# Performance work log

Measured on AMD Instinct MI355X. Metric: run time of the kernel, lower is better.

The kernel has to match this reference:

```python
import jax, jax.numpy as jnp
import numpy as np

B, T, E, H, D = 2, 2048, 1024, 16, 64
ROPE_BASE = 10000.0


def project(x, k):
    # Lift to Lorentz hyperboloid with curvature magnitude K=exp(k): <lx,lx>_L = -K
    K = jnp.exp(k)
    x0 = jnp.sqrt(K + jnp.sum(x * x, axis=-1, keepdims=True))
    return jnp.concatenate([x0, x], axis=-1)


def layer_norm(x, w, b, eps=1e-5):
    m = jnp.mean(x, axis=-1, keepdims=True)
    v = jnp.mean((x - m) ** 2, axis=-1, keepdims=True)
    return (x - m) * jax.lax.rsqrt(v + eps) * w + b


def setup_inputs() -> dict:
    key = jax.random.key(0)
    ks = jax.random.split(key, 8)
    s = 0.02
    return dict(
        x=jax.random.normal(ks[0], (B, T, E), jnp.float32),
        block_curvature=jnp.asarray(1.0, jnp.float32),
        mlp_curvature=jnp.asarray(1.0, jnp.float32),
        attn_curvatures=jnp.ones((1, H, 1, 1), jnp.float32),
        w_qkv=jax.random.normal(ks[1], (E + 1, 3 * E), jnp.float32) * s,
        w_attn_proj=jax.random.normal(ks[2], ((D + 1) * H, E), jnp.float32) * s,
        b_attn_proj=jnp.zeros((E,), jnp.float32),
        w_mlp_expand=jax.random.normal(ks[3], (E + 1, 4 * E + 3), jnp.float32) * s,
        b_mlp_expand=jnp.zeros((4 * E + 3,), jnp.float32),
        w_mlp_shrink=jax.random.normal(ks[4], (4 * (E + 1), E), jnp.float32) * s,
        b_mlp_shrink=jnp.zeros((E,), jnp.float32),
        ln_w=jnp.ones((E,), jnp.float32),
        ln_b=jnp.zeros((E,), jnp.float32),
    )


def _block(x, block_curvature, mlp_curvature, attn_curvatures, w_qkv,
           w_attn_proj, b_attn_proj, w_mlp_expand, b_mlp_expand,
           w_mlp_shrink, b_mlp_shrink, ln_w, ln_b):
    Bq, Tq = x.shape[0], x.shape[1]
    lx = project(x, block_curvature)  # (B,T,E+1)

    def block_norm(l):
        return project(layer_norm(l[..., 1:], ln_w, ln_b), block_curvature)

    def skip(l, f):  # hyperbolic skip: add space parts, re-lift
        return project(l[..., 1:] + f[..., 1:], block_curvature)

    def attn(l):
        qkv = l @ w_qkv  # (B,T,3E)
        q, k, v = jnp.split(qkv, 3, axis=-1)
        q = q.reshape(Bq, Tq, H, D)
        k = k.reshape(Bq, Tq, H, D)
        v = v.reshape(Bq, Tq, H, D)
        half = D // 2
        inv_freq = 1.0 / (ROPE_BASE ** (jnp.arange(0, D, 2, dtype=jnp.float32) / D))
        freqs = jnp.arange(Tq, dtype=jnp.float32)[:, None] * inv_freq[None, :]
        cos = jnp.cos(freqs)[None, :, None, :]  # (1,T,1,D/2)
        sin = jnp.sin(freqs)[None, :, None, :]

        def rope(t):
            t1, t2 = t[..., :half], t[..., half:]
            return jnp.concatenate([t1 * cos + t2 * sin, -t1 * sin + t2 * cos], axis=-1)

        q = rope(q).transpose(0, 2, 1, 3)  # (B,H,T,D)
        k = rope(k).transpose(0, 2, 1, 3)
        v = v.transpose(0, 2, 1, 3)
        K = jnp.exp(attn_curvatures)  # (1,H,1,1) per-head curvature
        qt = jnp.sqrt(K + jnp.sum(q * q, axis=-1, keepdims=True))  # time coord (B,H,T,1)
        kt = jnp.sqrt(K + jnp.sum(k * k, axis=-1, keepdims=True))
        lv = project(v, attn_curvatures)  # (B,H,T,D+1)
        # Lorentz inner product without materializing (B,H,T,T,D+1)
        inner = jnp.einsum('bhtd,bhsd->bhts', q, k) - qt * jnp.swapaxes(kt, -1, -2)
        ratio = jnp.maximum(-inner / K, 1.0 + 1e-7)
        dis = jnp.sqrt(K) * jnp.arccosh(ratio)  # (B,H,T,T)
        causal = jnp.tril(jnp.ones((Tq, Tq), dtype=bool))
        w = jnp.where(causal, -dis, -jnp.inf)  # neg_dis attention weight + causal bias
        aw = jax.nn.softmax(w, axis=-1)
        o = jnp.einsum('bhts,bhse->bhte', aw, lv)  # (B,H,T,D+1)
        lnorm2 = o[..., :1] ** 2 - jnp.sum(o[..., 1:] ** 2, axis=-1, keepdims=True)
        hn = jnp.sqrt(jnp.maximum(lnorm2, 1e-12))  # Lorentz norm
        o = o * jnp.sqrt(K) / hn  # renormalize back onto hyperboloid
        o = o.transpose(0, 2, 1, 3).reshape(Bq, Tq, H * (D + 1))
        return project(o @ w_attn_proj + b_attn_proj, block_curvature)

    def mlp(l):
        h = project(l @ w_mlp_expand + b_mlp_expand, mlp_curvature)[..., 1:]  # (B,T,4E+3)
        h = jax.nn.gelu(h, approximate=False)
        h = project(h, mlp_curvature)  # (B,T,4(E+1))
        return project(h @ w_mlp_shrink + b_mlp_shrink, block_curvature)

    lx = skip(lx, attn(block_norm(lx)))
    lx = skip(lx, mlp(block_norm(lx)))
    return lx


def reference(x, block_curvature, mlp_curvature, attn_curvatures, w_qkv,
              w_attn_proj, b_attn_proj, w_mlp_expand, b_mlp_expand,
              w_mlp_shrink, b_mlp_shrink, ln_w, ln_b):
    return _block(x, block_curvature, mlp_curvature, attn_curvatures, w_qkv,
                  w_attn_proj, b_attn_proj, w_mlp_expand, b_mlp_expand,
                  w_mlp_shrink, b_mlp_shrink, ln_w, ln_b)
```

## Files before the change

### kernel.cpp

```cpp
#include <hip/hip_runtime.h>
#include <math.h>

#define MM   4096
#define TT   2048
#define HH   16

typedef __bf16 bf16x8 __attribute__((ext_vector_type(8)));
typedef float f32x4 __attribute__((ext_vector_type(4)));

__device__ __forceinline__ void g2l16(const void* g, void* l) {
    __builtin_amdgcn_global_load_lds(
        (__attribute__((address_space(1))) void*)g,
        (__attribute__((address_space(3))) void*)l, 16, 0, 0);
}

#if __has_builtin(__builtin_amdgcn_exp2f)
__device__ __forceinline__ float fexp2(float x) { return __builtin_amdgcn_exp2f(x); }
#else
__device__ __forceinline__ float fexp2(float x) { return exp2f(x); }
#endif
#if __has_builtin(__builtin_amdgcn_logf)
__device__ __forceinline__ float flog2(float x) { return __builtin_amdgcn_logf(x); }
#else
__device__ __forceinline__ float flog2(float x) { return log2f(x); }
#endif
#if __has_builtin(__builtin_amdgcn_sqrtf)
__device__ __forceinline__ float fsqrt_(float x) { return __builtin_amdgcn_sqrtf(x); }
#else
__device__ __forceinline__ float fsqrt_(float x) { return sqrtf(x); }
#endif
#if __has_builtin(__builtin_amdgcn_rcpf)
__device__ __forceinline__ float frcp_(float x) { return __builtin_amdgcn_rcpf(x); }
#else
__device__ __forceinline__ float frcp_(float x) { return 1.0f / x; }
#endif
#if __has_builtin(__builtin_amdgcn_rsqf)
__device__ __forceinline__ float frsq_(float x) { return __builtin_amdgcn_rsqf(x); }
#else
__device__ __forceinline__ float frsq_(float x) { return rsqrtf(x); }
#endif

__device__ __forceinline__ float blockSum256(float v, volatile float* sb) {
    int lane = threadIdx.x & 63, w = threadIdx.x >> 6;
#pragma unroll
    for (int o = 32; o; o >>= 1) v += __shfl_xor(v, o);
    if (lane == 0) sb[w] = v;
    __syncthreads();
    v = sb[0] + sb[1] + sb[2] + sb[3];
    __syncthreads();
    return v;
}

__global__ __launch_bounds__(256) void block_norm_bf_k(
    const float* __restrict__ in, int ld,
    __bf16* __restrict__ out,
    const float* __restrict__ lw, const float* __restrict__ lb,
    const float* __restrict__ curv)
{
    int row = blockIdx.x;
    const float* x = in + (size_t)row * ld;
    __bf16* o = out + (size_t)row * 1056;
    __shared__ float sb[4];
    int tid = threadIdx.x;
    float v[4]; float s1 = 0.f, s2 = 0.f;
#pragma unroll
    for (int r = 0; r < 4; r++) {
        float t = x[tid + 256 * r];
        v[r] = t; s1 += t; s2 += t * t;
    }
    s1 = blockSum256(s1, sb);
    s2 = blockSum256(s2, sb);
    float mean = s1 * (1.f / 1024.f);
    float var  = s2 * (1.f / 1024.f) - mean * mean;
    float rs = rsqrtf(var + 1e-5f);
    float y[4]; float ssq = 0.f;
#pragma unroll
    for (int r = 0; r < 4; r++) {
        int i = tid + 256 * r;
        float t = (v[r] - mean) * rs * lw[i] + lb[i];
        y[r] = t; ssq += t * t;
    }
    ssq = blockSum256(ssq, sb);
#pragma unroll
    for (int r = 0; r < 4; r++) o[1 + tid + 256 * r] = (__bf16)y[r];
    if (tid == 0) o[0] = (__bf16)sqrtf(expf(*curv) + ssq);
    if (tid < 31) o[1025 + tid] = (__bf16)0.f;
}

__global__ __launch_bounds__(256) void row_x0_k(
    float* __restrict__ buf, int stride, int n, const float* __restrict__ curv)
{
    int row = blockIdx.x;
    float* base = buf + (size_t)row * stride;
    __shared__ float sb[4];
    float s = 0.f;
    for (int i = threadIdx.x; i < n; i += 256) { float t = base[1 + i]; s += t * t; }
    s = blockSum256(s, sb);
    if (threadIdx.x == 0) base[0] = sqrtf(expf(*curv) + s);
}

__global__ __launch_bounds__(256) void row_x0_bf_k(
    __bf16* __restrict__ buf, const float* __restrict__ curv)
{
    int row = blockIdx.x;
    __bf16* base = buf + (size_t)row * 4128;
    __shared__ float sb[4];
    float s = 0.f;
    for (int i = threadIdx.x; i < 4099; i += 256) { float t = (float)base[1 + i]; s += t * t; }
    s = blockSum256(s, sb);
    if (threadIdx.x == 0) base[0] = (__bf16)sqrtf(expf(*curv) + s);
    if (threadIdx.x < 28) base[4100 + threadIdx.x] = (__bf16)0.f;
}

__global__ __launch_bounds__(256) void wt_k(
    const float* __restrict__ W, int K, int N,
    __bf16* __restrict__ Wt, int Kp)
{
    __shared__ float s[32][33];
    int tx = threadIdx.x & 31, ty = threadIdx.x >> 5;
    int k0 = blockIdx.x * 32, n0 = blockIdx.y * 32;
#pragma unroll
    for (int r = 0; r < 4; r++) {
        int k = k0 + ty + 8 * r, n = n0 + tx;
        s[ty + 8 * r][tx] = (k < K && n < N) ? W[(size_t)k * N + n] : 0.f;
    }
    __syncthreads();
#pragma unroll
    for (int r = 0; r < 4; r++) {
        int n = n0 + ty + 8 * r, k = k0 + tx;
        if (n < N) Wt[(size_t)n * Kp + k] = (__bf16)s[tx][ty + 8 * r];
    }
}

template<bool BIAS, bool GELU, bool SKIP, bool OUTBF>
__global__ __launch_bounds__(256) void mgemm_k(
    const __bf16* __restrict__ A, int lda,
    const __bf16* __restrict__ Bt, int ldb,
    const float* __restrict__ bias,
    const float* __restrict__ skip, int ldskip,
    void* __restrict__ Cout, int ldc,
    int N, int Kp)
{
    __shared__ __bf16 sA[128 * 32];
    __shared__ __bf16 sB[128 * 32];
    int tid = threadIdx.x;
    int w = tid >> 6, lane = tid & 63;
    int m0 = blockIdx.y * 128, n0 = blockIdx.x * 128;
    const __bf16* Ab = A + (size_t)m0 * lda;
    const __bf16* Bb = Bt + (size_t)n0 * ldb;

    f32x4 zero = {0.f, 0.f, 0.f, 0.f};
    f32x4 acc[4][4];
#pragma unroll
    for (int i = 0; i < 4; i++)
#pragma unroll
        for (int j = 0; j < 4; j++) acc[i][j] = zero;

    int mw = (w & 1) * 64, nw = (w >> 1) * 64;
    int lr = lane & 15, lq = lane >> 4;
    int fko = lq * 8;

    int r1 = tid >> 2, kk1 = (tid & 3) * 8;
    int r2 = (tid + 256) >> 2, kk2 = (tid & 3) * 8;
    __bf16* lA1 = &sA[(size_t)(w * 64) * 8];
    __bf16* lA2 = &sA[(size_t)(256 + w * 64) * 8];
    __bf16* lB1 = &sB[(size_t)(w * 64) * 8];
    __bf16* lB2 = &sB[(size_t)(256 + w * 64) * 8];

    for (int k0 = 0; k0 < Kp; k0 += 32) {
        g2l16(Ab + (size_t)r1 * lda + k0 + kk1, lA1);
        g2l16(Ab + (size_t)r2 * lda + k0 + kk2, lA2);
        g2l16(Bb + (size_t)r1 * ldb + k0 + kk1, lB1);
        g2l16(Bb + (size_t)r2 * ldb + k0 + kk2, lB2);
        __syncthreads();
        bf16x8 af[4], bf[4];
#pragma unroll
        for (int i = 0; i < 4; i++) af[i] = *(const bf16x8*)&sA[(mw + i * 16 + lr) * 32 + fko];
#pragma unroll
        for (int j = 0; j < 4; j++) bf[j] = *(const bf16x8*)&sB[(nw + j * 16 + lr) * 32 + fko];
#pragma unroll
        for (int i = 0; i < 4; i++)
#pragma unroll
            for (int j = 0; j < 4; j++)
                acc[i][j] = __builtin_amdgcn_mfma_f32_16x16x32_bf16(af[i], bf[j], acc[i][j], 0, 0, 0);
        __syncthreads();
    }

#pragma unroll
    for (int j = 0; j < 4; j++) {
        int n = n0 + nw + j * 16 + lr;
        if (n < N) {
            float bv = BIAS ? bias[n] : 0.f;
#pragma unroll
            for (int i = 0; i < 4; i++) {
#pragma unroll
                for (int r = 0; r < 4; r++) {
                    int m = m0 + mw + i * 16 + lq * 4 + r;
                    float v = acc[i][j][r] + bv;
                    if (GELU) v = 0.5f * v * (1.f + erff(v * 0.70710678118654752f));
                    if (SKIP) v += skip[(size_t)m * ldskip + n];
                    if (OUTBF) ((__bf16*)Cout)[(size_t)m * ldc + n] = (__bf16)v;
                    else       ((float*)Cout)[(size_t)m * ldc + n] = v;
                }
            }
        }
    }
}

template<bool BIAS, bool GELU, bool SKIP>
__global__ __launch_bounds__(256) void mgemm64_k(
    const __bf16* __restrict__ A, int lda,
    const __bf16* __restrict__ Bt, int ldb,
    const float* __restrict__ bias,
    const float* __restrict__ skip, int ldskip,
    float* __restrict__ Cout, int ldc,
    int N, int Kp)
{
    __shared__ __bf16 sA[128 * 32];
    __shared__ __bf16 sB[64 * 32];
    int tid = threadIdx.x;
    int w = tid >> 6, lane = tid & 63;
    int m0 = blockIdx.y * 128, n0 = blockIdx.x * 64;
    const __bf16* Ab = A + (size_t)m0 * lda;
    const __bf16* Bb = Bt + (size_t)n0 * ldb;

    f32x4 zero = {0.f, 0.f, 0.f, 0.f};
    f32x4 acc[4][2];
#pragma unroll
    for (int i = 0; i < 4; i++) { acc[i][0] = zero; acc[i][1] = zero; }

    int mw = (w & 1) * 64, nw = (w >> 1) * 32;
    int lr = lane & 15, lq = lane >> 4;
    int fko = lq * 8;

    int rA = tid >> 2, kkA = (tid & 3) * 8;
    __bf16* lA1 = &sA[(size_t)(w * 64) * 8];
    __bf16* lA2 = &sA[(size_t)(256 + w * 64) * 8];
    __bf16* lB  = &sB[(size_t)(w * 64) * 8];

    for (int k0 = 0; k0 < Kp; k0 += 32) {
        g2l16(Ab + (size_t)rA * lda + k0 + kkA, lA1);
        g2l16(Ab + (size_t)(rA + 64) * lda + k0 + kkA, lA2);
        g2l16(Bb + (size_t)rA * ldb + k0 + kkA, lB);
        __syncthreads();
        bf16x8 af[4], bf[2];
#pragma unroll
        for (int i = 0; i < 4; i++) af[i] = *(const bf16x8*)&sA[(mw + i * 16 + lr) * 32 + fko];
#pragma unroll
        for (int j = 0; j < 2; j++) bf[j] = *(const bf16x8*)&sB[(nw + j * 16 + lr) * 32 + fko];
#pragma unroll
        for (int i = 0; i < 4; i++)
#pragma unroll
            for (int j = 0; j < 2; j++)
                acc[i][j] = __builtin_amdgcn_mfma_f32_16x16x32_bf16(af[i], bf[j], acc[i][j], 0, 0, 0);
        __syncthreads();
    }

#pragma unroll
    for (int j = 0; j < 2; j++) {
        int n = n0 + nw + j * 16 + lr;
        if (n < N) {
            float bv = BIAS ? bias[n] : 0.f;
#pragma unroll
            for (int i = 0; i < 4; i++) {
#pragma unroll
                for (int r = 0; r < 4; r++) {
                    int m = m0 + mw + i * 16 + lq * 4 + r;
                    float v = acc[i][j][r] + bv;
                    if (GELU) v = 0.5f * v * (1.f + erff(v * 0.70710678118654752f));
                    if (SKIP) v += skip[(size_t)m * ldskip + n];
                    Cout[(size_t)m * ldc + n] = v;
                }
            }
        }
    }
}

__global__ __launch_bounds__(256) void rope_k(
    float* __restrict__ QKV, const float* __restrict__ curv,
    float* __restrict__ qt, float* __restrict__ kt,
    __bf16* __restrict__ Kb, __bf16* __restrict__ Obf)
{
    int row = blockIdx.x;
    int b = row >> 11, t = row & (TT - 1);
    int wv = threadIdx.x >> 6, d = threadIdx.x & 63;
    int j = d & 31;
    float fr = (float)t * powf(10000.0f, -(float)(2 * j) / 64.0f);
    float cv = cosf(fr), sv = sinf(fr);
    float sgn = (d < 32) ? sv : -sv;
    for (int h = wv; h < HH; h += 4) {
        float Kh = expf(curv[h]);
        float* base = QKV + (size_t)row * 3072 + h * 64;
        float q = base[d], k = base[1024 + d];
        float qp = __shfl_xor(q, 32);
        float kp = __shfl_xor(k, 32);
        float qr = q * cv + qp * sgn;
        float kr = k * cv + kp * sgn;
        base[d] = qr;
        size_t oidx = ((size_t)(b * HH + h) * TT + t);
        Kb[oidx * 64 + d] = (__bf16)kr;
        float sq = qr * qr, sk = kr * kr;
#pragma unroll
        for (int o = 32; o; o >>= 1) {
            sq += __shfl_xor(sq, o);
            sk += __shfl_xor(sk, o);
        }
        if (d == 0) {
            qt[oidx] = sqrtf(Kh + sq);
            kt[oidx] = sqrtf(Kh + sk);
        }
    }
    if (threadIdx.x < 16) Obf[(size_t)row * 1056 + 1040 + threadIdx.x] = (__bf16)0.f;
}

__global__ __launch_bounds__(256) void vtrans_k(
    const float* __restrict__ QKV, const float* __restrict__ curv,
    __bf16* __restrict__ Vtb, float* __restrict__ vt)
{
    __shared__ float sT[64 * 65];
    int bh = blockIdx.y; int h = bh & (HH - 1); int b = bh >> 4;
    int t0 = blockIdx.x * 64;
    int tid = threadIdx.x, w = tid >> 6, lane = tid & 63;
    float Kh = expf(curv[h]);
    const float* vbase = QKV + (size_t)(b * TT + t0) * 3072 + 2048 + h * 64;
#pragma unroll 4
    for (int i = 0; i < 16; i++) {
        int tr = w * 16 + i;
        float v = vbase[(size_t)tr * 3072 + lane];
        sT[lane * 65 + tr] = v;
        float s = v * v;
#pragma unroll
        for (int o = 32; o; o >>= 1) s += __shfl_xor(s, o);
        if (lane == 0) vt[(size_t)bh * TT + t0 + tr] = sqrtf(Kh + s);
    }
    __syncthreads();
    int d = tid >> 2, seg = tid & 3;
    const float* r = &sT[d * 65 + seg * 16];
    bf16x8 o0, o1;
#pragma unroll
    for (int i = 0; i < 8; i++) { o0[i] = (__bf16)r[i]; o1[i] = (__bf16)r[8 + i]; }
    __bf16* dst = Vtb + ((size_t)bh * 64 + d) * TT + t0 + seg * 16;
    *(bf16x8*)dst = o0;
    *(bf16x8*)(dst + 8) = o1;
}

__global__ __launch_bounds__(256, 4) void flash_k(
    const float* __restrict__ QKV,
    const __bf16* __restrict__ Kb, const __bf16* __restrict__ Vtb,
    const float* __restrict__ qt, const float* __restrict__ kt,
    const float* __restrict__ vt,
    const float* __restrict__ curv,
    __bf16* __restrict__ O)
{
    __shared__ __bf16 sK[4096];
    __shared__ __bf16 sVt[4096];
    __shared__ __bf16 sP[4 * 16 * 72];
    __shared__ float skt[64], svt[64];

    int bh = blockIdx.x; int h = bh & (HH - 1); int b = bh >> 4;
    int pi = blockIdx.y;
    float Kh = expf(curv[h]);
    float sqKh = sqrtf(Kh), msqK = -sqKh, invKh = 1.0f / Kh;
    const float* tok = QKV + (size_t)b * TT * 3072 + h * 64;
    const char* KbB = (const char*)Kb + (size_t)bh * TT * 128;
    const char* VtB = (const char*)Vtb + (size_t)bh * 64 * (TT * 2);
    const float* qtp = qt + (size_t)bh * TT;
    const float* ktp = kt + (size_t)bh * TT;
    const float* vtp = vt + (size_t)bh * TT;

    int tid = threadIdx.x;
    int w = tid >> 6, lane = tid & 63;
    int m = lane & 15, quad = lane >> 4;
    int qA = pi * 32, qB = (63 - pi) * 32;
    int myBase = (w < 2) ? (qA + 16 * w) : (qB + 16 * (w - 2));
    int myJmax = (myBase + 15) >> 6;
    int blockJmax = (qB + 31) >> 6;
    __bf16* sPw = &sP[w * 16 * 72];

    bf16x8 qhi[2], qlo[2];
    {
        const float* qrow = tok + (size_t)(myBase + m) * 3072;
#pragma unroll
        for (int ks = 0; ks < 2; ks++) {
            const float* s = qrow + quad * 8 + 32 * ks;
            float4 f0 = *(const float4*)s;
            float4 f1 = *(const float4*)(s + 4);
            float fa[8] = {f0.x, f0.y, f0.z, f0.w, f1.x, f1.y, f1.z, f1.w};
#pragma unroll
            for (int jj = 0; jj < 8; jj++) {
                __bf16 hv = (__bf16)fa[jj];
                qhi[ks][jj] = hv;
                qlo[ks][jj] = (__bf16)(fa[jj] - (float)hv);
            }
        }
    }
    float qtv[4]; int qg[4];
#pragma unroll
    for (int r = 0; r < 4; r++) { qg[r] = myBase + quad * 4 + r; qtv[r] = qtp[qg[r]]; }

    f32x4 zero = {0.f, 0.f, 0.f, 0.f};
    f32x4 accO[4];
#pragma unroll
    for (int nt = 0; nt < 4; nt++) accO[nt] = zero;
    float lsumr[4] = {}, o0r[4] = {};

    char* sKb  = (char*)sK  + w * 1024;
    char* sVb  = (char*)sVt + w * 1024;

    for (int j = 0; j <= blockJmax; ++j) {
        int sb = j << 6;
        __syncthreads();
        {
            const char* kg = KbB + (size_t)(sb + lane) * 128 + w * 16;
            g2l16(kg,      sKb);
            g2l16(kg + 64, sKb + 4096);
            const char* vg = VtB + (size_t)lane * (TT * 2) + sb * 2 + w * 16;
            g2l16(vg,      sVb);
            g2l16(vg + 64, sVb + 4096);
        }
        if (tid < 64) skt[tid] = ktp[sb + tid];
        else if (tid < 128) svt[tid - 64] = vtp[sb + tid - 64];
        __syncthreads();

        if (j > myJmax) continue;

        f32x4 accS[4];
#pragma unroll
        for (int nt = 0; nt < 4; nt++) accS[nt] = zero;
#pragma unroll
        for (int nt = 0; nt < 4; nt++) {
#pragma unroll
            for (int ksp = 0; ksp < 2; ksp++) {
                bf16x8 bk = *(const bf16x8*)&sK[((ksp * 4 + quad) * 64 + nt * 16 + m) * 8];
                accS[nt] = __builtin_amdgcn_mfma_f32_16x16x32_bf16(qhi[ksp], bk, accS[nt], 0, 0, 0);
                accS[nt] = __builtin_amdgcn_mfma_f32_16x16x32_bf16(qlo[ksp], bk, accS[nt], 0, 0, 0);
            }
        }
#pragma unroll
        for (int nt = 0; nt < 4; nt++) {
            int col = nt * 16 + m;
            int sglob = sb + col;
            float ktv = skt[col], vtv = svt[col];
#pragma unroll
            for (int r = 0; r < 4; r++) {
                float dot = accS[nt][r];
                float rdiff = fmaf(qtv[r], ktv, -dot);
                float ratio = fmaxf(rdiff * invKh, 1.0f + 1e-7f);
                float y = ratio + fsqrt_(fmaf(ratio, ratio, -1.0f));
                float pv = fexp2(msqK * flog2(y));
                float p = (sglob <= qg[r]) ? pv : 0.0f;
                lsumr[r] += p;
                o0r[r] = fmaf(p, vtv, o0r[r]);
                sPw[(quad * 4 + r) * 72 + col] = (__bf16)p;
            }
        }
        __asm__ volatile("s_waitcnt lgkmcnt(0)" ::: "memory");
#pragma unroll
        for (int ksp = 0; ksp < 2; ksp++) {
            bf16x8 aP = *(const bf16x8*)&sPw[m * 72 + ksp * 32 + quad * 8];
#pragma unroll
            for (int nt = 0; nt < 4; nt++) {
                bf16x8 bV = *(const bf16x8*)&sVt[((ksp * 4 + quad) * 64 + nt * 16 + m) * 8];
                accO[nt] = __builtin_amdgcn_mfma_f32_16x16x32_bf16(aP, bV, accO[nt], 0, 0, 0);
            }
        }
    }

#pragma unroll
    for (int r = 0; r < 4; r++) {
#pragma unroll
        for (int off = 1; off < 16; off <<= 1) {
            lsumr[r] += __shfl_xor(lsumr[r], off);
            o0r[r]   += __shfl_xor(o0r[r], off);
        }
    }
#pragma unroll
    for (int r = 0; r < 4; r++) {
        float inv = frcp_(lsumr[r]);
        float o0f = o0r[r] * inv;
        float ov[4]; float part = 0.f;
#pragma unroll
        for (int nt = 0; nt < 4; nt++) { float t = accO[nt][r] * inv; ov[nt] = t; part += t * t; }
        part += __shfl_xor(part, 1);
        part += __shfl_xor(part, 2);
        part += __shfl_xor(part, 4);
        part += __shfl_xor(part, 8);
        float scale = sqKh * frsq_(fmaxf(o0f * o0f - part, 1e-12f));
        size_t orow = (size_t)(b * TT + qg[r]) * 1056 + h * 65;
        if (m == 0) O[orow] = (__bf16)(o0f * scale);
#pragma unroll
        for (int nt = 0; nt < 4; nt++) O[orow + 1 + nt * 16 + m] = (__bf16)(ov[nt] * scale);
    }
}

extern "C" void kernel_launch(void* const* d_in, const int* in_sizes, int n_in,
                              void* d_out, int out_size, void* d_ws, size_t ws_size,
                              hipStream_t stream) {
    const float* x    = (const float*)d_in[0];
    const float* bc   = (const float*)d_in[1];
    const float* mc   = (const float*)d_in[2];
    const float* ac   = (const float*)d_in[3];
    const float* w_qkv = (const float*)d_in[4];
    const float* w_ap  = (const float*)d_in[5];
    const float* b_ap  = (const float*)d_in[6];
    const float* w_me  = (const float*)d_in[7];
    const float* b_me  = (const float*)d_in[8];
    const float* w_ms  = (const float*)d_in[9];
    const float* b_ms  = (const float*)d_in[10];
    const float* lnw  = (const float*)d_in[11];
    const float* lnb  = (const float*)d_in[12];
    float* out = (float*)d_out;
    float* ws  = (float*)d_ws;

    float* R      = ws;
    float* qkvbuf = R;
    float* X2     = R;
    __bf16* h_bf  = (__bf16*)(R + 4194304);
    float* p      = R + 12648448;
    __bf16* ln_bf = (__bf16*)p;  p += 2162688;
    __bf16* o_bf  = (__bf16*)p;  p += 2162688;
    __bf16* qkvT  = (__bf16*)p;  p += 1622016;
    __bf16* apT   = (__bf16*)p;  p += 540672;
    float*  meT_f = p;           p += 2164272;
    float*  msT_f = p;           p += 2113536;
    float* Qt = p;               p += 2 * HH * TT;
    float* Kt = p;               p += 2 * HH * TT;
    float* Vt = p;
    __bf16* meT = (__bf16*)meT_f;
    __bf16* msT = (__bf16*)msT_f;
    __bf16* Kb  = (__bf16*)meT_f;
    __bf16* Vtb = (__bf16*)msT_f;

    wt_k<<<dim3(33, 96),  256, 0, stream>>>(w_qkv, 1025, 3072, qkvT, 1056);
    wt_k<<<dim3(33, 32),  256, 0, stream>>>(w_ap,  1040, 1024, apT,  1056);

    block_norm_bf_k<<<MM, 256, 0, stream>>>(x, 1024, ln_bf, lnw, lnb, bc);
    mgemm_k<false, false, false, false><<<dim3(24, 32), 256, 0, stream>>>(
        ln_bf, 1056, qkvT, 1056, nullptr, nullptr, 0, qkvbuf, 3072, 3072, 1056);
    rope_k<<<MM, 256, 0, stream>>>(qkvbuf, ac, Qt, Kt, Kb, o_bf);
    vtrans_k<<<dim3(32, 32), 256, 0, stream>>>(qkvbuf, ac, Vtb, Vt);
    flash_k<<<dim3(2 * HH, 32), 256, 0, stream>>>(qkvbuf, Kb, Vtb, Qt, Kt, Vt, ac, o_bf);
    wt_k<<<dim3(33, 129), 256, 0, stream>>>(w_me,  1025, 4099, meT, 1056);
    wt_k<<<dim3(129, 32), 256, 0, stream>>>(w_ms,  4100, 1024, msT, 4128);
    mgemm64_k<true, false, true><<<dim3(16, 32), 256, 0, stream>>>(
        o_bf, 1056, apT, 1056, b_ap, x, 1024, X2, 1024, 1024, 1056);
    block_norm_bf_k<<<MM, 256, 0, stream>>>(X2, 1024, ln_bf, lnw, lnb, bc);
    mgemm_k<true, true, false, true><<<dim3(33, 32), 256, 0, stream>>>(
        ln_bf, 1056, meT, 1056, b_me, nullptr, 0, (void*)(h_bf + 1), 4128, 4099, 1056);
    row_x0_bf_k<<<MM, 256, 0, stream>>>(h_bf, mc);
    mgemm64_k<true, false, true><<<dim3(16, 32), 256, 0, stream>>>(
        h_bf, 4128, msT, 4128, b_ms, X2, 1024, out + 1, 1025, 1024, 4128);
    row_x0_k<<<MM, 256, 0, stream>>>(out, 1025, 1024, bc);
}
```

Measured before the change: 531.8 us.

## Replace 128x128 GEMM with double-buffered 256x256 swizzled MFMA kernel

Replaces the 128x128 single-buffered bf16 MFMA GEMM with a 512-thread 256x256-tile kernel. The new kernel uses a K-step of 64, double-buffered LDS prefetch via global_load_lds, an XOR-swizzled LDS layout, and setprio around the MFMA bursts. Leading dimensions are padded to multiples of 64 (1088, 4224) to fit the wider K-step, so the workspace offsets change. The 3 leftover MLP-expand columns (4096-4098) are computed by a small dot-product kernel fused into the x0 row reduction, so the big GEMM grid tiles N evenly. The aim is more data reuse and latency hiding in the QKV and MLP-expand GEMMs, at the cost of higher LDS and register use and extra padding traffic.

```diff
diff --git a/kernel.cpp b/kernel.cpp
--- a/kernel.cpp
+++ b/kernel.cpp
@@ -53,13 +53,13 @@
 
 __global__ __launch_bounds__(256) void block_norm_bf_k(
     const float* __restrict__ in, int ld,
-    __bf16* __restrict__ out,
+    __bf16* __restrict__ out, int ldo,
     const float* __restrict__ lw, const float* __restrict__ lb,
     const float* __restrict__ curv)
 {
     int row = blockIdx.x;
     const float* x = in + (size_t)row * ld;
-    __bf16* o = out + (size_t)row * 1056;
+    __bf16* o = out + (size_t)row * ldo;
     __shared__ float sb[4];
     int tid = threadIdx.x;
     float v[4]; float s1 = 0.f, s2 = 0.f;
@@ -84,7 +84,7 @@
 #pragma unroll
     for (int r = 0; r < 4; r++) o[1 + tid + 256 * r] = (__bf16)y[r];
     if (tid == 0) o[0] = (__bf16)sqrtf(expf(*curv) + ssq);
-    if (tid < 31) o[1025 + tid] = (__bf16)0.f;
+    if (tid < ldo - 1025) o[1025 + tid] = (__bf16)0.f;
 }
 
 __global__ __launch_bounds__(256) void row_x0_k(
@@ -99,17 +99,48 @@
     if (threadIdx.x == 0) base[0] = sqrtf(expf(*curv) + s);
 }
 
-__global__ __launch_bounds__(256) void row_x0_bf_k(
-    __bf16* __restrict__ buf, const float* __restrict__ curv)
+__global__ __launch_bounds__(256) void row_x0_tail_k(
+    __bf16* __restrict__ h,
+    const __bf16* __restrict__ ln,
+    const __bf16* __restrict__ Bt,
+    const float* __restrict__ bias,
+    const float* __restrict__ curv)
 {
     int row = blockIdx.x;
-    __bf16* base = buf + (size_t)row * 4128;
+    __bf16* base = h + (size_t)row * 4224;
+    const __bf16* lnr = ln + (size_t)row * 1088;
+    const __bf16* B0 = Bt + (size_t)4096 * 1088;
+    const __bf16* B1 = Bt + (size_t)4097 * 1088;
+    const __bf16* B2 = Bt + (size_t)4098 * 1088;
     __shared__ float sb[4];
+    float d0 = 0.f, d1 = 0.f, d2 = 0.f;
+    for (int i = threadIdx.x; i < 1088; i += 256) {
+        float a = (float)lnr[i];
+        d0 += a * (float)B0[i];
+        d1 += a * (float)B1[i];
+        d2 += a * (float)B2[i];
+    }
+    d0 = blockSum256(d0, sb);
+    d1 = blockSum256(d1, sb);
+    d2 = blockSum256(d2, sb);
+    float t3[3] = {d0 + bias[4096], d1 + bias[4097], d2 + bias[4098]};
+    float ssq_t = 0.f;
+#pragma unroll
+    for (int j = 0; j < 3; j++) {
+        float v = t3[j];
+        v = 0.5f * v * (1.f + erff(v * 0.70710678118654752f));
+        t3[j] = v; ssq_t += v * v;
+    }
+    if (threadIdx.x == 0) {
+        base[1 + 4096] = (__bf16)t3[0];
+        base[1 + 4097] = (__bf16)t3[1];
+        base[1 + 4098] = (__bf16)t3[2];
+    }
     float s = 0.f;
-    for (int i = threadIdx.x; i < 4099; i += 256) { float t = (float)base[1 + i]; s += t * t; }
-    s = blockSum256(s, sb);
+    for (int i = threadIdx.x; i < 4096; i += 256) { float t = (float)base[1 + i]; s += t * t; }
+    s = blockSum256(s, sb) + ssq_t;
     if (threadIdx.x == 0) base[0] = (__bf16)sqrtf(expf(*curv) + s);
-    if (threadIdx.x < 28) base[4100 + threadIdx.x] = (__bf16)0.f;
+    if (threadIdx.x < 124) base[4100 + threadIdx.x] = (__bf16)0.f;
 }
 
 __global__ __launch_bounds__(256) void wt_k(
@@ -132,73 +163,155 @@
     }
 }
 
-template<bool BIAS, bool GELU, bool SKIP, bool OUTBF>
-__global__ __launch_bounds__(256) void mgemm_k(
+template<bool BIAS, bool GELU, bool OUTBF>
+__global__ __launch_bounds__(512, 2) void mgemm256_k(
     const __bf16* __restrict__ A, int lda,
-    const __bf16* __restrict__ Bt, int ldb,
+    const __bf16* __restrict__ Bt, int ldb, int NB,
     const float* __restrict__ bias,
-    const float* __restrict__ skip, int ldskip,
     void* __restrict__ Cout, int ldc,
     int N, int Kp)
 {
-    __shared__ __bf16 sA[128 * 32];
-    __shared__ __bf16 sB[128 * 32];
-    int tid = threadIdx.x;
-    int w = tid >> 6, lane = tid & 63;
-    int m0 = blockIdx.y * 128, n0 = blockIdx.x * 128;
-    const __bf16* Ab = A + (size_t)m0 * lda;
-    const __bf16* Bb = Bt + (size_t)n0 * ldb;
+    __shared__ __bf16 sAB[65536];
+    const int tid = threadIdx.x;
+    const int w = tid >> 6, lane = tid & 63;
+    const int wm = w >> 2, wn = w & 3;
+    const int lr = lane & 15, lq = lane >> 4;
+    const int m0 = blockIdx.y * 256, n0 = blockIdx.x * 256;
+
+    const int rr  = tid >> 3;
+    const int csw = ((tid & 7) ^ (rr & 7)) << 3;
+    const __bf16* gA[4]; const __bf16* gB[4];
+#pragma unroll
+    for (int c = 0; c < 4; c++) {
+        gA[c] = A + (size_t)(m0 + c * 64 + rr) * lda + csw;
+        int rb = n0 + c * 64 + rr; rb = (rb < NB) ? rb : (NB - 1);
+        gB[c] = Bt + (size_t)rb * ldb + csw;
+    }
+    __bf16* lA = sAB + (w << 9);
+    __bf16* lB = sAB + 32768 + (w << 9);
+
+    const int off0 = (lq * 8) ^ ((lr & 7) << 3);
+    const int off1 = off0 ^ 32;
+    const int arow = wm * 128 + lr;
+    const int brow = wn * 64 + lr;
 
     f32x4 zero = {0.f, 0.f, 0.f, 0.f};
-    f32x4 acc[4][4];
-#pragma unroll
-    for (int i = 0; i < 4; i++)
+    f32x4 acc[8][4];
+#pragma unroll
+    for (int i = 0; i < 8; i++)
 #pragma unroll
         for (int j = 0; j < 4; j++) acc[i][j] = zero;
 
-    int mw = (w & 1) * 64, nw = (w >> 1) * 64;
-    int lr = lane & 15, lq = lane >> 4;
-    int fko = lq * 8;
-
-    int r1 = tid >> 2, kk1 = (tid & 3) * 8;
-    int r2 = (tid + 256) >> 2, kk2 = (tid & 3) * 8;
-    __bf16* lA1 = &sA[(size_t)(w * 64) * 8];
-    __bf16* lA2 = &sA[(size_t)(256 + w * 64) * 8];
-    __bf16* lB1 = &sB[(size_t)(w * 64) * 8];
-    __bf16* lB2 = &sB[(size_t)(256 + w * 64) * 8];
-
-    for (int k0 = 0; k0 < Kp; k0 += 32) {
-        g2l16(Ab + (size_t)r1 * lda + k0 + kk1, lA1);
-        g2l16(Ab + (size_t)r2 * lda + k0 + kk2, lA2);
-        g2l16(Bb + (size_t)r1 * ldb + k0 + kk1, lB1);
-        g2l16(Bb + (size_t)r2 * ldb + k0 + kk2, lB2);
-        __syncthreads();
-        bf16x8 af[4], bf[4];
-#pragma unroll
-        for (int i = 0; i < 4; i++) af[i] = *(const bf16x8*)&sA[(mw + i * 16 + lr) * 32 + fko];
-#pragma unroll
-        for (int j = 0; j < 4; j++) bf[j] = *(const bf16x8*)&sB[(nw + j * 16 + lr) * 32 + fko];
-#pragma unroll
-        for (int i = 0; i < 4; i++)
-#pragma unroll
-            for (int j = 0; j < 4; j++)
-                acc[i][j] = __builtin_amdgcn_mfma_f32_16x16x32_bf16(af[i], bf[j], acc[i][j], 0, 0, 0);
-        __syncthreads();
+#pragma unroll
+    for (int c = 0; c < 4; c++) {
+        g2l16(gA[c], lA + c * 4096);
+        g2l16(gB[c], lB + c * 4096);
+    }
+    asm volatile("s_waitcnt vmcnt(0)" ::: "memory");
+    __builtin_amdgcn_s_barrier();
+
+    const int NT = Kp >> 6;
+    for (int kt = 0; kt < NT; ++kt) {
+        const int cur = kt & 1;
+        const __bf16* pA = sAB + cur * 16384;
+        const __bf16* pB = sAB + 32768 + cur * 16384;
+        bf16x8 af[4][2], bfr[4][2];
+
+        if (kt + 1 < NT) {
+            const int ko = (kt + 1) << 6;
+            __bf16* dA = lA + (cur ^ 1) * 16384;
+            __bf16* dB = lB + (cur ^ 1) * 16384;
+#pragma unroll
+            for (int c = 0; c < 4; c++) {
+                g2l16(gA[c] + ko, dA + c * 4096);
+                g2l16(gB[c] + ko, dB + c * 4096);
+            }
+        }
+#pragma unroll
+        for (int i = 0; i < 4; i++) {
+            const __bf16* r = pA + (arow + i * 16) * 64;
+            af[i][0] = *(const bf16x8*)(r + off0);
+            af[i][1] = *(const bf16x8*)(r + off1);
+        }
+#pragma unroll
+        for (int j = 0; j < 2; j++) {
+            const __bf16* r = pB + (brow + j * 16) * 64;
+            bfr[j][0] = *(const bf16x8*)(r + off0);
+            bfr[j][1] = *(const bf16x8*)(r + off1);
+        }
+        __builtin_amdgcn_s_barrier();
+        __builtin_amdgcn_s_setprio(1);
+#pragma unroll
+        for (int ks = 0; ks < 2; ks++)
+#pragma unroll
+            for (int i = 0; i < 4; i++)
+#pragma unroll
+                for (int j = 0; j < 2; j++)
+                    acc[i][j] = __builtin_amdgcn_mfma_f32_16x16x32_bf16(af[i][ks], bfr[j][ks], acc[i][j], 0, 0, 0);
+        __builtin_amdgcn_s_setprio(0);
+        __builtin_amdgcn_s_barrier();
+
+#pragma unroll
+        for (int j = 2; j < 4; j++) {
+            const __bf16* r = pB + (brow + j * 16) * 64;
+            bfr[j][0] = *(const bf16x8*)(r + off0);
+            bfr[j][1] = *(const bf16x8*)(r + off1);
+        }
+        __builtin_amdgcn_s_barrier();
+        __builtin_amdgcn_s_setprio(1);
+#pragma unroll
+        for (int ks = 0; ks < 2; ks++)
+#pragma unroll
+            for (int i = 0; i < 4; i++)
+#pragma unroll
+                for (int j = 2; j < 4; j++)
+                    acc[i][j] = __builtin_amdgcn_mfma_f32_16x16x32_bf16(af[i][ks], bfr[j][ks], acc[i][j], 0, 0, 0);
+        __builtin_amdgcn_s_setprio(0);
+        __builtin_amdgcn_s_barrier();
+
+#pragma unroll
+        for (int i = 0; i < 4; i++) {
+            const __bf16* r = pA + (arow + 64 + i * 16) * 64;
+            af[i][0] = *(const bf16x8*)(r + off0);
+            af[i][1] = *(const bf16x8*)(r + off1);
+        }
+        __builtin_amdgcn_s_barrier();
+        __builtin_amdgcn_s_setprio(1);
+#pragma unroll
+        for (int ks = 0; ks < 2; ks++)
+#pragma unroll
+            for (int i = 0; i < 4; i++)
+#pragma unroll
+                for (int j = 0; j < 2; j++)
+                    acc[4 + i][j] = __builtin_amdgcn_mfma_f32_16x16x32_bf16(af[i][ks], bfr[j][ks], acc[4 + i][j], 0, 0, 0);
+        __builtin_amdgcn_s_setprio(0);
+        __builtin_amdgcn_s_barrier();
+
+        __builtin_amdgcn_s_setprio(1);
+#pragma unroll
+        for (int ks = 0; ks < 2; ks++)
+#pragma unroll
+            for (int i = 0; i < 4; i++)
+#pragma unroll
+                for (int j = 2; j < 4; j++)
+                    acc[4 + i][j] = __builtin_amdgcn_mfma_f32_16x16x32_bf16(af[i][ks], bfr[j][ks], acc[4 + i][j], 0, 0, 0);
+        __builtin_amdgcn_s_setprio(0);
+        asm volatile("s_waitcnt vmcnt(0) lgkmcnt(0)" ::: "memory");
+        __builtin_amdgcn_s_barrier();
     }
 
 #pragma unroll
     for (int j = 0; j < 4; j++) {
-        int n = n0 + nw + j * 16 + lr;
+        const int n = n0 + wn * 64 + j * 16 + lr;
         if (n < N) {
-            float bv = BIAS ? bias[n] : 0.f;
-#pragma unroll
-            for (int i = 0; i < 4; i++) {
+            const float bv = BIAS ? bias[n] : 0.f;
+#pragma unroll
+            for (int i = 0; i < 8; i++) {
 #pragma unroll
                 for (int r = 0; r < 4; r++) {
-                    int m = m0 + mw + i * 16 + lq * 4 + r;
+                    const int m = m0 + wm * 128 + i * 16 + lq * 4 + r;
                     float v = acc[i][j][r] + bv;
                     if (GELU) v = 0.5f * v * (1.f + erff(v * 0.70710678118654752f));
-                    if (SKIP) v += skip[(size_t)m * ldskip + n];
                     if (OUTBF) ((__bf16*)Cout)[(size_t)m * ldc + n] = (__bf16)v;
                     else       ((float*)Cout)[(size_t)m * ldc + n] = v;
                 }
@@ -516,13 +629,13 @@
     float* qkvbuf = R;
     float* X2     = R;
     __bf16* h_bf  = (__bf16*)(R + 4194304);
-    float* p      = R + 12648448;
-    __bf16* ln_bf = (__bf16*)p;  p += 2162688;
+    float* p      = R + 12845056;
+    __bf16* ln_bf = (__bf16*)p;  p += 2228224;
     __bf16* o_bf  = (__bf16*)p;  p += 2162688;
-    __bf16* qkvT  = (__bf16*)p;  p += 1622016;
+    __bf16* qkvT  = (__bf16*)p;  p += 1671168;
     __bf16* apT   = (__bf16*)p;  p += 540672;
-    float*  meT_f = p;           p += 2164272;
-    float*  msT_f = p;           p += 2113536;
+    float*  meT_f = p;           p += 2229856;
+    float*  msT_f = p;           p += 2162688;
     float* Qt = p;               p += 2 * HH * TT;
     float* Kt = p;               p += 2 * HH * TT;
     float* Vt = p;
@@ -531,24 +644,24 @@
     __bf16* Kb  = (__bf16*)meT_f;
     __bf16* Vtb = (__bf16*)msT_f;
 
-    wt_k<<<dim3(33, 96),  256, 0, stream>>>(w_qkv, 1025, 3072, qkvT, 1056);
+    wt_k<<<dim3(34, 96),  256, 0, stream>>>(w_qkv, 1025, 3072, qkvT, 1088);
     wt_k<<<dim3(33, 32),  256, 0, stream>>>(w_ap,  1040, 1024, apT,  1056);
 
-    block_norm_bf_k<<<MM, 256, 0, stream>>>(x, 1024, ln_bf, lnw, lnb, bc);
-    mgemm_k<false, false, false, false><<<dim3(24, 32), 256, 0, stream>>>(
-        ln_bf, 1056, qkvT, 1056, nullptr, nullptr, 0, qkvbuf, 3072, 3072, 1056);
+    block_norm_bf_k<<<MM, 256, 0, stream>>>(x, 1024, ln_bf, 1088, lnw, lnb, bc);
+    mgemm256_k<false, false, false><<<dim3(12, 16), 512, 0, stream>>>(
+        ln_bf, 1088, qkvT, 1088, 3072, nullptr, qkvbuf, 3072, 3072, 1088);
     rope_k<<<MM, 256, 0, stream>>>(qkvbuf, ac, Qt, Kt, Kb, o_bf);
     vtrans_k<<<dim3(32, 32), 256, 0, stream>>>(qkvbuf, ac, Vtb, Vt);
     flash_k<<<dim3(2 * HH, 32), 256, 0, stream>>>(qkvbuf, Kb, Vtb, Qt, Kt, Vt, ac, o_bf);
-    wt_k<<<dim3(33, 129), 256, 0, stream>>>(w_me,  1025, 4099, meT, 1056);
-    wt_k<<<dim3(129, 32), 256, 0, stream>>>(w_ms,  4100, 1024, msT, 4128);
+    wt_k<<<dim3(34, 129), 256, 0, stream>>>(w_me,  1025, 4099, meT, 1088);
+    wt_k<<<dim3(132, 32), 256, 0, stream>>>(w_ms,  4100, 1024, msT, 4224);
     mgemm64_k<true, false, true><<<dim3(16, 32), 256, 0, stream>>>(
         o_bf, 1056, apT, 1056, b_ap, x, 1024, X2, 1024, 1024, 1056);
-    block_norm_bf_k<<<MM, 256, 0, stream>>>(X2, 1024, ln_bf, lnw, lnb, bc);
-    mgemm_k<true, true, false, true><<<dim3(33, 32), 256, 0, stream>>>(
-        ln_bf, 1056, meT, 1056, b_me, nullptr, 0, (void*)(h_bf + 1), 4128, 4099, 1056);
-    row_x0_bf_k<<<MM, 256, 0, stream>>>(h_bf, mc);
+    block_norm_bf_k<<<MM, 256, 0, stream>>>(X2, 1024, ln_bf, 1088, lnw, lnb, bc);
+    mgemm256_k<true, true, true><<<dim3(16, 16), 512, 0, stream>>>(
+        ln_bf, 1088, meT, 1088, 4099, b_me, (void*)(h_bf + 1), 4224, 4099, 1088);
+    row_x0_tail_k<<<MM, 256, 0, stream>>>(h_bf, ln_bf, meT, b_me, mc);
     mgemm64_k<true, false, true><<<dim3(16, 32), 256, 0, stream>>>(
-        h_bf, 4128, msT, 4128, b_ms, X2, 1024, out + 1, 1025, 1024, 4128);
+        h_bf, 4224, msT, 4224, b_ms, X2, 1024, out + 1, 1025, 1024, 4224);
     row_x0_k<<<MM, 256, 0, stream>>>(out, 1025, 1024, bc);
 }
```

After: 511.2 us. 3.9% less time.
